# Kernel optimization log

Measured on AMD Instinct MI355X. Metric: run time of the kernel, lower is better.

The kernel has to match this reference:

```python
import jax, jax.numpy as jnp
import numpy as np

NUM_HEADS = 4
NUM_GROUPS = 8
EPS = 1e-5


def setup_inputs() -> dict:
    key = jax.random.key(0)
    ks = jax.random.split(key, 4)
    b, c, h, w = 16, 512, 32, 32
    x = jax.random.normal(ks[0], (b, c, h, w), dtype=jnp.float32)
    norm_gamma = jnp.ones((c,), dtype=jnp.float32)
    norm_beta = jnp.zeros((c,), dtype=jnp.float32)
    qkv_w = jax.random.normal(ks[1], (3 * c, c), dtype=jnp.float32) * (c ** -0.5)
    qkv_b = jnp.zeros((3 * c,), dtype=jnp.float32)
    proj_w = jax.random.normal(ks[2], (c, c), dtype=jnp.float32) * (c ** -0.5)
    proj_b = jnp.zeros((c,), dtype=jnp.float32)
    return {"x": x, "norm_gamma": norm_gamma, "norm_beta": norm_beta,
            "qkv_w": qkv_w, "qkv_b": qkv_b, "proj_w": proj_w, "proj_b": proj_b}


def reference(x, norm_gamma, norm_beta, qkv_w, qkv_b, proj_w, proj_b):
    b, c, h, w = x.shape
    nh = NUM_HEADS
    dh = c // nh
    n = h * w
    # GroupNorm(8, c): normalize over (c/G, h, w) within each group, biased var
    xg = x.reshape(b, NUM_GROUPS, -1)
    mu = jnp.mean(xg, axis=-1, keepdims=True)
    var = jnp.var(xg, axis=-1, keepdims=True)
    xn = ((xg - mu) * jax.lax.rsqrt(var + EPS)).reshape(b, c, h, w)
    xn = xn * norm_gamma[:, None, None] + norm_beta[:, None, None]
    # QKV 1x1 conv == channel matmul
    qkv = jnp.einsum('oc,bchw->bohw', qkv_w, xn) + qkv_b[:, None, None]
    q, k, v = jnp.split(qkv, 3, axis=1)  # each [b, c, h, w]

    def to_heads(t):  # [b, c, h, w] -> [b, nh, n, dh]
        return t.reshape(b, nh, dh, n).transpose(0, 1, 3, 2)

    q, k, v = to_heads(q), to_heads(k), to_heads(v)
    scale = dh ** -0.5
    attn = jax.nn.softmax(jnp.einsum('bhnd,bhmd->bhnm', q, k) * scale, axis=-1)
    out = jnp.einsum('bhnm,bhmd->bhnd', attn, v)  # [b, nh, n, dh]
    out = out.transpose(0, 1, 3, 2).reshape(b, c, h, w)
    out = jnp.einsum('oc,bchw->bohw', proj_w, out) + proj_b[:, None, None]
    return x + out
```

## Files before the change

### kernel.cpp

```cpp
#include <hip/hip_runtime.h>

typedef unsigned short u16;
typedef unsigned int   u32;

typedef __attribute__((ext_vector_type(8)))  short bf16x8;
typedef __attribute__((ext_vector_type(16))) float f32x16;
typedef __attribute__((ext_vector_type(2)))  unsigned int u32x2;
#define MFMA32(a, b, c) __builtin_amdgcn_mfma_f32_32x32x16_bf16(a, b, c, 0, 0, 0)

__device__ __forceinline__ float bf2f(u16 h) { return __uint_as_float(((u32)h) << 16); }
__device__ __forceinline__ u16 f2bf(float f) {
  u32 u = __float_as_uint(f);
  u += 0x7fffu + ((u >> 16) & 1u);
  return (u16)(u >> 16);
}
__device__ __forceinline__ void unpack8(uint4 u, float* f) {
  f[0] = __uint_as_float(u.x << 16); f[1] = __uint_as_float(u.x & 0xffff0000u);
  f[2] = __uint_as_float(u.y << 16); f[3] = __uint_as_float(u.y & 0xffff0000u);
  f[4] = __uint_as_float(u.z << 16); f[5] = __uint_as_float(u.z & 0xffff0000u);
  f[6] = __uint_as_float(u.w << 16); f[7] = __uint_as_float(u.w & 0xffff0000u);
}
__device__ __forceinline__ void unpack4(uint2 u, float* f) {
  f[0] = __uint_as_float(u.x << 16); f[1] = __uint_as_float(u.x & 0xffff0000u);
  f[2] = __uint_as_float(u.y << 16); f[3] = __uint_as_float(u.y & 0xffff0000u);
}

template <bool F>
__device__ __forceinline__ void load8(const void* p, size_t idx, float* f) {
  if constexpr (F) {
    const float4* q = (const float4*)((const float*)p + idx);
    float4 a = q[0], b = q[1];
    f[0] = a.x; f[1] = a.y; f[2] = a.z; f[3] = a.w;
    f[4] = b.x; f[5] = b.y; f[6] = b.z; f[7] = b.w;
  } else {
    unpack8(*(const uint4*)((const u16*)p + idx), f);
  }
}
template <bool F>
__device__ __forceinline__ void load4(const void* p, size_t idx, float* f) {
  if constexpr (F) {
    float4 a = *(const float4*)((const float*)p + idx);
    f[0] = a.x; f[1] = a.y; f[2] = a.z; f[3] = a.w;
  } else {
    unpack4(*(const uint2*)((const u16*)p + idx), f);
  }
}
template <bool F>
__device__ __forceinline__ float load1(const void* p, size_t idx) {
  if constexpr (F) return ((const float*)p)[idx];
  else return bf2f(((const u16*)p)[idx]);
}

__device__ __forceinline__ void gl2lds16(const void* g, void* l) {
  __builtin_amdgcn_global_load_lds(
      (const __attribute__((address_space(1))) void*)g,
      (__attribute__((address_space(3))) void*)l, 16, 0, 0);
}

__global__ void detect_dtype(const void* __restrict__ x, int* __restrict__ flag) {
  if (threadIdx.x == 0 && blockIdx.x == 0) {
    const u32* p = (const u32*)x;
    int sane = 0;
    for (int i = 0; i < 256; ++i) {
      u32 e = (p[i] >> 7) & 0xFFu;
      sane += (e >= 100u && e <= 150u) ? 1 : 0;
    }
    *flag = (sane < 192) ? 1 : 0;
  }
}

__global__ void signal_ws(u16* __restrict__ out, int n) {
  int i = blockIdx.x * 256 + threadIdx.x;
  if (i < n) out[i] = 0x42C8;
}

#define SM_SCALE 0.08838834764831843f
#define QSC 0.12751743f


__global__ void __launch_bounds__(256) wconv_rt(const void* __restrict__ qkvw,
                                                const void* __restrict__ qkvb,
                                                u16* __restrict__ dst,
                                                const int* __restrict__ flag) {
  const bool F = (flag[0] != 0);
  int i = (blockIdx.x * 256 + threadIdx.x) * 8;
  if (i >= 787968) return;
  if (!F) {
    uint4 v = (i < 786432) ? *(const uint4*)((const u16*)qkvw + i)
                           : *(const uint4*)((const u16*)qkvb + (i - 786432));
    *(uint4*)(dst + i) = v;
  } else {
    const float* src = (i < 786432) ? ((const float*)qkvw + i)
                                    : ((const float*)qkvb + (i - 786432));
    float f[8];
    float4 a = *(const float4*)src, b = *(const float4*)(src + 4);
    f[0]=a.x; f[1]=a.y; f[2]=a.z; f[3]=a.w; f[4]=b.x; f[5]=b.y; f[6]=b.z; f[7]=b.w;
    u32 w0 = (u32)f2bf(f[0]) | ((u32)f2bf(f[1]) << 16);
    u32 w1 = (u32)f2bf(f[2]) | ((u32)f2bf(f[3]) << 16);
    u32 w2 = (u32)f2bf(f[4]) | ((u32)f2bf(f[5]) << 16);
    u32 w3 = (u32)f2bf(f[6]) | ((u32)f2bf(f[7]) << 16);
    *(uint4*)(dst + i) = make_uint4(w0, w1, w2, w3);
  }
}

template <bool F>
__device__ __forceinline__ void gn_stats2_body(const void* __restrict__ x,
                                               float* __restrict__ part,
                                               int g, int b, int half, int tid,
                                               float* ssum, float* ssq) {
  const size_t base = (size_t)(b * 512 + g * 64 + half * 32) * 1024;
  float sum = 0.f, sq = 0.f;
  for (int i = tid; i < 4096; i += 256) {
    float f[8]; load8<F>(x, base + (size_t)i * 8, f);
#pragma unroll
    for (int m = 0; m < 8; ++m) { sum += f[m]; sq += f[m] * f[m]; }
  }
  ssum[tid] = sum; ssq[tid] = sq; __syncthreads();
  for (int off = 128; off > 0; off >>= 1) {
    if (tid < off) { ssum[tid] += ssum[tid + off]; ssq[tid] += ssq[tid + off]; }
    __syncthreads();
  }
  if (tid == 0) {
    part[(b * 8 + g) * 4 + half * 2 + 0] = ssum[0];
    part[(b * 8 + g) * 4 + half * 2 + 1] = ssq[0];
  }
}

__global__ void __launch_bounds__(256) gn_stats2(const void* __restrict__ x,
                                                 float* __restrict__ part,
                                                 const int* __restrict__ flag) {
  __shared__ float ssum[256], ssq[256];
  const int g = blockIdx.x, b = blockIdx.y, half = blockIdx.z, tid = threadIdx.x;
  if (flag[0] != 0) gn_stats2_body<true >(x, part, g, b, half, tid, ssum, ssq);
  else              gn_stats2_body<false>(x, part, g, b, half, tid, ssum, ssq);
}

template <bool F>
__device__ __forceinline__ void gn_apply_body(
    const void* __restrict__ x, const void* __restrict__ gamma,
    const void* __restrict__ beta, const float* __restrict__ part,
    u16* __restrict__ xT, int chunk, int b, int tid,
    float* scb, float* bsb, float (*Tf)[64][65]) {
  const int s0 = chunk * 64;
  for (int c = tid; c < 512; c += 256) {
    int gg = c >> 6;
    const float* p = part + (b * 8 + gg) * 4;
    float sum = p[0] + p[2], sq = p[1] + p[3];
    float mu  = sum * (1.f / 65536.f);
    float var = sq * (1.f / 65536.f) - mu * mu;
    float s = load1<F>(gamma, c) * rsqrtf(var + 1e-5f);
    scb[c] = s;
    bsb[c] = load1<F>(beta, c) - mu * s;
  }
  __syncthreads();

  for (int gb = 0; gb < 8; ++gb) {
    const int pb = gb & 1;
#pragma unroll
    for (int half = 0; half < 2; ++half) {
      int idx = tid + half * 256;
      int c_loc = idx >> 3, s8 = (idx & 7) * 8;
      int c = gb * 64 + c_loc;
      float f[8];
      load8<F>(x, (size_t)(b * 512 + c) * 1024 + s0 + s8, f);
      float sm = scb[c], ba = bsb[c];
#pragma unroll
      for (int m = 0; m < 8; ++m) Tf[pb][s8 + m][c_loc] = f[m] * sm + ba;
    }
    __syncthreads();
#pragma unroll
    for (int half = 0; half < 2; ++half) {
      int idx = tid + half * 256;
      int s_loc = idx >> 3, c8 = (idx & 7) * 8;
      u32 pk[4];
#pragma unroll
      for (int m = 0; m < 4; ++m)
        pk[m] = (u32)f2bf(Tf[pb][s_loc][c8 + 2 * m]) |
                ((u32)f2bf(Tf[pb][s_loc][c8 + 2 * m + 1]) << 16);
      *(uint4*)(xT + (size_t)(b * 1024 + s0 + s_loc) * 512 + gb * 64 + c8) =
          make_uint4(pk[0], pk[1], pk[2], pk[3]);
    }
  }
}

__global__ void __launch_bounds__(256) gn_apply(const void* __restrict__ x,
                                                const void* __restrict__ gamma,
                                                const void* __restrict__ beta,
                                                const float* __restrict__ part,
                                                u16* __restrict__ xT,
                                                const int* __restrict__ flag) {
  __shared__ float scb[512], bsb[512];
  __shared__ float Tf[2][64][65];
  const int chunk = blockIdx.x, b = blockIdx.y, tid = threadIdx.x;
  if (flag[0] != 0) gn_apply_body<true >(x, gamma, beta, part, xT, chunk, b, tid, scb, bsb, Tf);
  else              gn_apply_body<false>(x, gamma, beta, part, xT, chunk, b, tid, scb, bsb, Tf);
}

__global__ void __launch_bounds__(256, 4)
gemm_qkv(const u16* __restrict__ xT, const u16* __restrict__ wbf,
         u16* __restrict__ qkT, u16* __restrict__ Vbuf) {
  const bool vrole = (blockIdx.y >= 8);
  const int n0 = blockIdx.x * 128;
  const int m0 = (vrole ? (int)blockIdx.y - 8 : (int)blockIdx.y) * 128;
  const int b  = blockIdx.z;
  __shared__ __align__(16) u16 At[8192];
  __shared__ __align__(16) u16 Bt[8192];
  const int tid = threadIdx.x;
  const int w = tid >> 6, lane = tid & 63;
  const int lo = lane & 31, hi = lane >> 5;
  const int wm = w >> 1, wn = w & 1;
  const u16* bias = wbf + 786432;
  const u16* Ab = vrole ? (wbf + 524288) : (xT + (size_t)b * 524288);
  const u16* Bb = vrole ? (xT + (size_t)b * 524288) : wbf;
  u16* outp = vrole ? (Vbuf + (size_t)b * 524288) : (qkT + (size_t)b * 1048576);
  const int srow = lane >> 3, spc = lane & 7;

  f32x16 cA[2][2];
#pragma unroll
  for (int i = 0; i < 2; ++i)
#pragma unroll
    for (int j = 0; j < 2; ++j)
#pragma unroll
      for (int r = 0; r < 16; ++r) cA[i][j][r] = 0.f;

  for (int kt = 0; kt < 8; ++kt) {
    const int kb = kt * 64;
#pragma unroll
    for (int c = 0; c < 4; ++c) {
      int grp = w * 4 + c;
      int row = grp * 8 + srow;
      int lc  = spc ^ (row & 7);
      gl2lds16(Ab + (size_t)(m0 + row) * 512 + kb + lc * 8, &At[grp * 512]);
      gl2lds16(Bb + (size_t)(n0 + row) * 512 + kb + lc * 8, &Bt[grp * 512]);
    }
    __syncthreads();
#pragma unroll
    for (int k16 = 0; k16 < 4; ++k16) {
      const int lc = k16 * 2 + hi;
      const int rA0 = wm * 64 + lo,  rA1 = rA0 + 32;
      const int rB0 = wn * 64 + lo,  rB1 = rB0 + 32;
      bf16x8 a0 = *(const bf16x8*)&At[rA0 * 64 + ((lc ^ (rA0 & 7)) << 3)];
      bf16x8 a1 = *(const bf16x8*)&At[rA1 * 64 + ((lc ^ (rA1 & 7)) << 3)];
      bf16x8 b0 = *(const bf16x8*)&Bt[rB0 * 64 + ((lc ^ (rB0 & 7)) << 3)];
      bf16x8 b1 = *(const bf16x8*)&Bt[rB1 * 64 + ((lc ^ (rB1 & 7)) << 3)];
      cA[0][0] = MFMA32(a0, b0, cA[0][0]);
      cA[0][1] = MFMA32(a0, b1, cA[0][1]);
      cA[1][0] = MFMA32(a1, b0, cA[1][0]);
      cA[1][1] = MFMA32(a1, b1, cA[1][1]);
    }
    __syncthreads();
  }

  float bcol[2] = {0.f, 0.f};
  if (!vrole) {
    bcol[0] = bf2f(bias[n0 + wn * 64 + lo]);
    bcol[1] = bf2f(bias[n0 + wn * 64 + 32 + lo]);
  }
#pragma unroll
  for (int mt = 0; mt < 2; ++mt)
#pragma unroll
    for (int nt = 0; nt < 2; ++nt) {
      const int nbase = n0 + wn * 64 + nt * 32;
#pragma unroll
      for (int r = 0; r < 16; ++r) {
        int m = m0 + wm * 64 + mt * 32 + (r & 3) + 8 * (r >> 2) + 4 * hi;
        int n = nbase + lo;
        float v = cA[mt][nt][r];
        if (!vrole) {
          v += bcol[nt];
          if (nbase < 512) v *= QSC;
        } else {
          v += bf2f(bias[1024 + m]);
        }
        outp[(size_t)m * 1024 + n] = f2bf(v);
      }
    }
}

template <bool F>
__device__ __forceinline__ void proj_body(const void* __restrict__ A,
                                          const u16* __restrict__ B,
                                          const void* __restrict__ bias,
                                          const void* __restrict__ resid,
                                          void* __restrict__ outp,
                                          int n0, int m0, int b, int tid,
                                          u16 (*At)[72], u16 (*Bt)[72]) {
  const int w = tid >> 6, lane = tid & 63;
  const int lo = lane & 31, hi = lane >> 5;
  const int wm = w >> 1, wn = w & 1;
  const size_t bBase = (size_t)b * 524288;

  f32x16 cA[2][2];
#pragma unroll
  for (int i = 0; i < 2; ++i)
#pragma unroll
    for (int j = 0; j < 2; ++j)
#pragma unroll
      for (int r = 0; r < 16; ++r) cA[i][j][r] = 0.f;

  for (int kt = 0; kt < 8; ++kt) {
#pragma unroll
    for (int i = 0; i < 4; ++i) {
      int idx = tid + i * 256;
      int row = idx >> 3, kc = (idx & 7) * 8;
      int k = kt * 64 + kc;
      {
        if constexpr (F) {
          float f[8]; load8<true>(A, (size_t)(m0 + row) * 512 + k, f);
          u32 w0 = (u32)f2bf(f[0]) | ((u32)f2bf(f[1]) << 16);
          u32 w1 = (u32)f2bf(f[2]) | ((u32)f2bf(f[3]) << 16);
          u32 w2 = (u32)f2bf(f[4]) | ((u32)f2bf(f[5]) << 16);
          u32 w3 = (u32)f2bf(f[6]) | ((u32)f2bf(f[7]) << 16);
          *(uint4*)&At[row][kc] = make_uint4(w0, w1, w2, w3);
        } else {
          *(uint4*)&At[row][kc] =
              *(const uint4*)((const u16*)A + (size_t)(m0 + row) * 512 + k);
        }
      }
      *(uint4*)&Bt[row][kc] =
          *(const uint4*)(B + bBase + (size_t)(n0 + row) * 512 + k);
    }
    __syncthreads();
#pragma unroll
    for (int k16 = 0; k16 < 4; ++k16) {
      const int ko = k16 * 16 + hi * 8;
      bf16x8 a0 = *(const bf16x8*)&At[wm * 64 + lo][ko];
      bf16x8 a1 = *(const bf16x8*)&At[wm * 64 + 32 + lo][ko];
      bf16x8 b0 = *(const bf16x8*)&Bt[wn * 64 + lo][ko];
      bf16x8 b1 = *(const bf16x8*)&Bt[wn * 64 + 32 + lo][ko];
      cA[0][0] = MFMA32(a0, b0, cA[0][0]);
      cA[0][1] = MFMA32(a0, b1, cA[0][1]);
      cA[1][0] = MFMA32(a1, b0, cA[1][0]);
      cA[1][1] = MFMA32(a1, b1, cA[1][1]);
    }
    __syncthreads();
  }

#pragma unroll
  for (int mt = 0; mt < 2; ++mt)
#pragma unroll
    for (int nt = 0; nt < 2; ++nt) {
#pragma unroll
      for (int r = 0; r < 16; ++r) {
        int m = m0 + wm * 64 + mt * 32 + (r & 3) + 8 * (r >> 2) + 4 * hi;
        int n = n0 + wn * 64 + nt * 32 + lo;
        float v = cA[mt][nt][r];
        v += load1<F>(bias, m);
        v += load1<F>(resid, bBase + (size_t)m * 1024 + n);
        size_t off = bBase + (size_t)m * 1024 + n;
        if constexpr (F) ((float*)outp)[off] = v;
        else             ((u16*)outp)[off] = f2bf(v);
      }
    }
}

__global__ void __launch_bounds__(256, 4)
proj_rt(const void* __restrict__ projw, const u16* __restrict__ aout,
        const void* __restrict__ projb, const void* __restrict__ x,
        void* __restrict__ outp, const int* __restrict__ flag) {
  __shared__ __align__(16) u16 At[128][72];
  __shared__ __align__(16) u16 Bt[128][72];
  const int n0 = blockIdx.x * 128, m0 = blockIdx.y * 128, b = blockIdx.z;
  if (flag[0] != 0) proj_body<true >(projw, aout, projb, x, outp, n0, m0, b, threadIdx.x, At, Bt);
  else              proj_body<false>(projw, aout, projb, x, outp, n0, m0, b, threadIdx.x, At, Bt);
}

__global__ void __launch_bounds__(256, 2) attn4(const u16* __restrict__ qkT,
                                                const u16* __restrict__ V,
                                                u16* __restrict__ aout) {
  const int bh = blockIdx.x;
  const int q0 = blockIdx.y * 128;
  const int b = bh >> 2, h = bh & 3;
  const u16* qt = qkT + (size_t)b * 1048576;
  const u16* vb = V + (size_t)b * 524288 + (size_t)(h * 128) * 1024;
  __shared__ __align__(16) u16 smem[32768];
  const int tid = threadIdx.x;
  const int w = tid >> 6, lane = tid & 63;
  const int lo = lane & 31, hi = lane >> 5;

#pragma unroll
  for (int c = 0; c < 8; ++c) {
    int grp = w * 8 + c;
    int row = grp * 4 + (lane >> 4);
    int lc  = (lane & 15) ^ (row & 7);
    gl2lds16(qt + (size_t)(q0 + row) * 1024 + h * 128 + lc * 8, &smem[grp * 512]);
  }
#pragma unroll
  for (int c = 0; c < 4; ++c) {
    int grp = w * 4 + c;
    { int row = grp * 4 + (lane >> 4);
      int lc  = (lane & 15) ^ (row & 7);
      gl2lds16(qt + (size_t)row * 1024 + 512 + h * 128 + lc * 8,
               &smem[16384 + grp * 512]); }
    { int row = grp * 8 + (lane >> 3);
      int lc  = (lane & 7) ^ (row & 7);
      gl2lds16(vb + (size_t)row * 1024 + lc * 8,
               &smem[16384 + 8192 + grp * 512]); }
  }
  __syncthreads();
  bf16x8 qf[8];
  {
    const int row = 32 * w + lo;
#pragma unroll
    for (int k16 = 0; k16 < 8; ++k16) {
      int lc = k16 * 2 + hi;
      qf[k16] = *(const bf16x8*)&smem[row * 128 + ((lc ^ (row & 7)) << 3)];
    }
  }
  __syncthreads();

  f32x16 o[4];
  float lp = 0.f;
#pragma unroll
  for (int dt = 0; dt < 4; ++dt)
#pragma unroll
    for (int r = 0; r < 16; ++r) o[dt][r] = 0.f;

  for (int kt = 0; kt < 16; ++kt) {
    const u16* rb = &smem[((kt & 1) ^ 1) << 14];
    u16* wbuf = &smem[(kt & 1) << 14];

    if (kt < 15) {
      const int k0n = (kt + 1) * 64;
#pragma unroll
      for (int c = 0; c < 4; ++c) {
        int grp = w * 4 + c;
        { int row = grp * 4 + (lane >> 4);
          int lc  = (lane & 15) ^ (row & 7);
          gl2lds16(qt + (size_t)(k0n + row) * 1024 + 512 + h * 128 + lc * 8,
                   wbuf + grp * 512); }
        { int row = grp * 8 + (lane >> 3);
          int lc  = (lane & 7) ^ (row & 7);
          gl2lds16(vb + (size_t)row * 1024 + k0n + lc * 8,
                   wbuf + 8192 + grp * 512); }
      }
    }

    f32x16 s0, s1;
#pragma unroll
    for (int r = 0; r < 16; ++r) { s0[r] = 0.f; s1[r] = 0.f; }
#pragma unroll
    for (int k16 = 0; k16 < 8; ++k16) {
      const int lc = k16 * 2 + hi;
      const int r0 = lo, r1 = lo + 32;
      bf16x8 kf0 = *(const bf16x8*)&rb[r0 * 128 + ((lc ^ (r0 & 7)) << 3)];
      bf16x8 kf1 = *(const bf16x8*)&rb[r1 * 128 + ((lc ^ (r1 & 7)) << 3)];
      s0 = MFMA32(kf0, qf[k16], s0);
      s1 = MFMA32(kf1, qf[k16], s1);
    }

#pragma unroll
    for (int r = 0; r < 16; ++r) {
      s0[r] = exp2f(s0[r]);
      s1[r] = exp2f(s1[r]);
      lp += s0[r] + s1[r];
    }

    bf16x8 pa[4];
#define MKPA(ps, rb0, dst) do {                                               \
      u32 qa0, qa1, qb0, qb1;                                                 \
      asm("v_cvt_pk_bf16_f32 %0, %1, %2" : "=v"(qa0)                          \
          : "v"((ps)[(rb0) + 0]), "v"((ps)[(rb0) + 1]));                      \
      asm("v_cvt_pk_bf16_f32 %0, %1, %2" : "=v"(qa1)                          \
          : "v"((ps)[(rb0) + 2]), "v"((ps)[(rb0) + 3]));                      \
      asm("v_cvt_pk_bf16_f32 %0, %1, %2" : "=v"(qb0)                          \
          : "v"((ps)[(rb0) + 4]), "v"((ps)[(rb0) + 5]));                      \
      asm("v_cvt_pk_bf16_f32 %0, %1, %2" : "=v"(qb1)                          \
          : "v"((ps)[(rb0) + 6]), "v"((ps)[(rb0) + 7]));                      \
      u32x2 r0 = __builtin_amdgcn_permlane32_swap(qa0, qb0, false, false);    \
      u32x2 r1 = __builtin_amdgcn_permlane32_swap(qa1, qb1, false, false);    \
      union { u32 u[4]; bf16x8 v8; } pk_;                                     \
      pk_.u[0] = r0[0]; pk_.u[1] = r1[0]; pk_.u[2] = r0[1]; pk_.u[3] = r1[1]; \
      dst = pk_.v8;                                                           \
    } while (0)
    MKPA(s0, 0, pa[0]);
    MKPA(s0, 8, pa[1]);
    MKPA(s1, 0, pa[2]);
    MKPA(s1, 8, pa[3]);
#undef MKPA

#pragma unroll
    for (int t = 0; t < 4; ++t) {
      const int lc = t * 2 + hi;
#pragma unroll
      for (int dt = 0; dt < 4; ++dt) {
        const int row = dt * 32 + lo;
        bf16x8 bv = *(const bf16x8*)&rb[8192 + row * 64 + ((lc ^ (row & 7)) << 3)];
        o[dt] = MFMA32(pa[t], bv, o[dt]);
      }
    }
    __syncthreads();
  }

  float linv = 1.f / (lp + __shfl_xor(lp, 32));
#pragma unroll
  for (int r = 0; r < 16; ++r) {
    int pat = (r & 3) + 8 * (r >> 2) + 4 * hi;
    float lr = __shfl(linv, pat);
    int q = q0 + 32 * w + pat;
    size_t base = (size_t)(b * 1024 + q) * 512 + h * 128;
    aout[base +  0 + lo] = f2bf(o[0][r] * lr);
    aout[base + 32 + lo] = f2bf(o[1][r] * lr);
    aout[base + 64 + lo] = f2bf(o[2][r] * lr);
    aout[base + 96 + lo] = f2bf(o[3][r] * lr);
  }
}


template <bool F>
__global__ void __launch_bounds__(256) gn_stats(const void* __restrict__ x,
                                                const void* __restrict__ gamma,
                                                const void* __restrict__ beta,
                                                float* __restrict__ sc,
                                                float* __restrict__ bs,
                                                const int* __restrict__ flag) {
  if ((flag[0] != 0) != F) return;
  const int g = blockIdx.x, b = blockIdx.y;
  const int tid = threadIdx.x;
  const size_t base = (size_t)(b * 512 + g * 64) * 1024;
  float sum = 0.f, sq = 0.f;
  for (int i = tid; i < 8192; i += 256) {
    float f[8]; load8<F>(x, base + (size_t)i * 8, f);
#pragma unroll
    for (int m = 0; m < 8; ++m) { sum += f[m]; sq += f[m] * f[m]; }
  }
  __shared__ float ssum[256], ssq[256];
  ssum[tid] = sum; ssq[tid] = sq; __syncthreads();
  for (int off = 128; off > 0; off >>= 1) {
    if (tid < off) { ssum[tid] += ssum[tid + off]; ssq[tid] += ssq[tid + off]; }
    __syncthreads();
  }
  if (tid < 64) {
    float mu  = ssum[0] * (1.f / 65536.f);
    float var = ssq[0] * (1.f / 65536.f) - mu * mu;
    int c = g * 64 + tid;
    float s = load1<F>(gamma, c) * rsqrtf(var + 1e-5f);
    sc[b * 512 + c] = s;
    bs[b * 512 + c] = load1<F>(beta, c) - mu * s;
  }
}

template <bool F, bool BEXT, bool FOUT>
__global__ void __launch_bounds__(256) gemm64(const void* __restrict__ A,
                                              const void* __restrict__ B,
                                              const float* __restrict__ sc,
                                              const float* __restrict__ bs,
                                              const void* __restrict__ bias,
                                              const void* __restrict__ resid,
                                              void* __restrict__ outp,
                                              int mrows, int donorm, int bstride,
                                              const int* __restrict__ flag) {
  if ((flag[0] != 0) != F) return;
  const int s0 = blockIdx.x * 64;
  const int o0 = blockIdx.y * 64;
  const int b  = blockIdx.z;
  __shared__ __align__(16) float At[64][36];
  __shared__ __align__(16) float Bt[64][36];
  const int tid = threadIdx.x;
  const int ty = tid >> 4, tx = tid & 15;
  const int i0 = ty * 4, j0 = tx * 4;
  const int arow = tid >> 2, akc = (tid & 3) * 8;
  const int brow = tid >> 3, bnc = (tid & 7) * 8;
  float acc[4][4] = {};

  for (int kt = 0; kt < 512; kt += 32) {
    float af[8];
    load8<F>(A, (size_t)(o0 + arow) * 512 + akc + kt, af);
    *(float4*)&At[arow][akc]     = make_float4(af[0], af[1], af[2], af[3]);
    *(float4*)&At[arow][akc + 4] = make_float4(af[4], af[5], af[6], af[7]);
    const int c = kt + brow;
    float bf[8];
    load8<(BEXT && F)>(B, (size_t)(b * bstride + c) * 1024 + s0 + bnc, bf);
    float smul = 1.f, badd = 0.f;
    if (donorm) { smul = sc[b * 512 + c]; badd = bs[b * 512 + c]; }
#pragma unroll
    for (int m = 0; m < 8; ++m) Bt[bnc + m][brow] = bf[m] * smul + badd;
    __syncthreads();
#pragma unroll
    for (int kq = 0; kq < 8; ++kq) {
      float4 a0 = *(const float4*)&At[i0 + 0][kq * 4];
      float4 a1 = *(const float4*)&At[i0 + 1][kq * 4];
      float4 a2 = *(const float4*)&At[i0 + 2][kq * 4];
      float4 a3 = *(const float4*)&At[i0 + 3][kq * 4];
      float4 c0 = *(const float4*)&Bt[j0 + 0][kq * 4];
      float4 c1 = *(const float4*)&Bt[j0 + 1][kq * 4];
      float4 c2 = *(const float4*)&Bt[j0 + 2][kq * 4];
      float4 c3 = *(const float4*)&Bt[j0 + 3][kq * 4];
#define DOT4(ii, jj, AV, CV) acc[ii][jj] += AV.x * CV.x + AV.y * CV.y + AV.z * CV.z + AV.w * CV.w;
      DOT4(0,0,a0,c0) DOT4(0,1,a0,c1) DOT4(0,2,a0,c2) DOT4(0,3,a0,c3)
      DOT4(1,0,a1,c0) DOT4(1,1,a1,c1) DOT4(1,2,a1,c2) DOT4(1,3,a1,c3)
      DOT4(2,0,a2,c0) DOT4(2,1,a2,c1) DOT4(2,2,a2,c2) DOT4(2,3,a2,c3)
      DOT4(3,0,a3,c0) DOT4(3,1,a3,c1) DOT4(3,2,a3,c2) DOT4(3,3,a3,c3)
#undef DOT4
    }
    __syncthreads();
  }
#pragma unroll
  for (int ii = 0; ii < 4; ++ii) {
    const int o = o0 + i0 + ii;
    const float bb = load1<F>(bias, o);
    float v[4];
#pragma unroll
    for (int jj = 0; jj < 4; ++jj) v[jj] = acc[ii][jj] + bb;
    if (resid) {
      float xf[4];
      load4<F>(resid, (size_t)(b * 512 + o) * 1024 + s0 + j0, xf);
#pragma unroll
      for (int jj = 0; jj < 4; ++jj) v[jj] += xf[jj];
    }
    const size_t ooff = (size_t)(b * mrows + o) * 1024 + s0 + j0;
    if constexpr (FOUT) {
      *(float4*)((float*)outp + ooff) = make_float4(v[0], v[1], v[2], v[3]);
    } else {
      uint2 pk;
      pk.x = (u32)f2bf(v[0]) | ((u32)f2bf(v[1]) << 16);
      pk.y = (u32)f2bf(v[2]) | ((u32)f2bf(v[3]) << 16);
      *(uint2*)((u16*)outp + ooff) = pk;
    }
  }
}

__global__ void __launch_bounds__(256, 2) attn_old(u16* __restrict__ qkv) {
  const int q0 = blockIdx.x * 128;
  const int bh = blockIdx.y;
  const int b = bh >> 2, h = bh & 3;
  u16* qp = qkv + (size_t)(b * 1536 + h * 128) * 1024;
  const u16* kp = qp + (size_t)512 * 1024;
  const u16* vp = qp + (size_t)1024 * 1024;
  __shared__ __align__(16) u16 Qt[128][136];
  __shared__ __align__(16) u16 Kt[32][136];
  __shared__ __align__(16) u16 Vt[128][40];
  __shared__ __align__(16) u16 Pt[128][40];
  const int tid = threadIdx.x;
  const int w = tid >> 6, lane = tid & 63;
  const int lo = lane & 31, hi = lane >> 5;

  for (int idx = tid; idx < 2048; idx += 256) {
    int d = idx >> 4, s8 = (idx & 15) * 8;
    uint4 qv = *(const uint4*)(qp + (size_t)d * 1024 + q0 + s8);
    const u16* qs = (const u16*)&qv;
#pragma unroll
    for (int m = 0; m < 8; ++m) Qt[s8 + m][d] = qs[m];
  }
  __syncthreads();
  bf16x8 qf[8];
#pragma unroll
  for (int kq = 0; kq < 8; ++kq)
    qf[kq] = *(const bf16x8*)&Qt[32 * w + lo][kq * 16 + hi * 8];

  f32x16 o0, o1, o2, o3;
  float lp[16];
#pragma unroll
  for (int r = 0; r < 16; ++r) { o0[r] = 0.f; o1[r] = 0.f; o2[r] = 0.f; o3[r] = 0.f; lp[r] = 0.f; }

  for (int kt = 0; kt < 32; ++kt) {
    const int k0 = kt * 32;
    __syncthreads();
    for (int idx = tid; idx < 512; idx += 256) {
      int d = idx >> 2, s8 = (idx & 3) * 8;
      uint4 kv = *(const uint4*)(kp + (size_t)d * 1024 + k0 + s8);
      const u16* ks = (const u16*)&kv;
#pragma unroll
      for (int m = 0; m < 8; ++m) Kt[s8 + m][d] = ks[m];
      *(uint4*)&Vt[d][s8] = *(const uint4*)(vp + (size_t)d * 1024 + k0 + s8);
    }
    __syncthreads();
    f32x16 acc;
#pragma unroll
    for (int r = 0; r < 16; ++r) acc[r] = 0.f;
#pragma unroll
    for (int kq = 0; kq < 8; ++kq) {
      bf16x8 bq = *(const bf16x8*)&Kt[lo][kq * 16 + hi * 8];
      acc = MFMA32(qf[kq], bq, acc);
    }
#pragma unroll
    for (int r = 0; r < 16; ++r) {
      float pe = __expf(acc[r] * SM_SCALE);
      lp[r] += pe;
      int row = (r & 3) + 8 * (r >> 2) + 4 * hi;
      Pt[32 * w + row][lo] = f2bf(pe);
    }
    __syncthreads();
#pragma unroll
    for (int kq2 = 0; kq2 < 2; ++kq2) {
      bf16x8 a2 = *(const bf16x8*)&Pt[32 * w + lo][kq2 * 16 + hi * 8];
      bf16x8 b0 = *(const bf16x8*)&Vt[ 0 + lo][kq2 * 16 + hi * 8];
      bf16x8 b1 = *(const bf16x8*)&Vt[32 + lo][kq2 * 16 + hi * 8];
      bf16x8 b2 = *(const bf16x8*)&Vt[64 + lo][kq2 * 16 + hi * 8];
      bf16x8 b3 = *(const bf16x8*)&Vt[96 + lo][kq2 * 16 + hi * 8];
      o0 = MFMA32(a2, b0, o0);
      o1 = MFMA32(a2, b1, o1);
      o2 = MFMA32(a2, b2, o2);
      o3 = MFMA32(a2, b3, o3);
    }
  }
#pragma unroll
  for (int r = 0; r < 16; ++r) {
    float su = lp[r];
    su += __shfl_xor(su, 1);  su += __shfl_xor(su, 2);
    su += __shfl_xor(su, 4);  su += __shfl_xor(su, 8);
    su += __shfl_xor(su, 16);
    float linv = 1.f / su;
    int row = (r & 3) + 8 * (r >> 2) + 4 * hi;
    int q = q0 + 32 * w + row;
    size_t base = (size_t)(b * 1536 + h * 128) * 1024 + q;
    qkv[base + (size_t)( 0 + lo) * 1024] = f2bf(o0[r] * linv);
    qkv[base + (size_t)(32 + lo) * 1024] = f2bf(o1[r] * linv);
    qkv[base + (size_t)(64 + lo) * 1024] = f2bf(o2[r] * linv);
    qkv[base + (size_t)(96 + lo) * 1024] = f2bf(o3[r] * linv);
  }
}

extern "C" void kernel_launch(void* const* d_in, const int* in_sizes, int n_in,
                              void* d_out, int out_size, void* d_ws, size_t ws_size,
                              hipStream_t stream) {
  const void* x     = d_in[0];
  const void* gamma = d_in[1];
  const void* beta  = d_in[2];
  const void* qkvw  = d_in[3];
  const void* qkvb  = d_in[4];
  const void* projw = d_in[5];
  const void* projb = d_in[6];

  char* ws = (char*)d_ws;
  const size_t MB = 1024 * 1024;
  const size_t FAST_NEED = 64 * MB + 64;
  const size_t OLD_NEED  = 48 * MB + 256 + 2 * 16 * 512 * 4;

  if (ws_size >= FAST_NEED) {
    u16* xT   = (u16*)ws;
    u16* qkT  = (u16*)(ws + 16 * MB);
    u16* Vbuf = (u16*)(ws + 48 * MB);
    int* flag = (int*)(ws + 64 * MB);
    u16* wbf  = (u16*)d_out;
    float* part = (float*)((char*)d_out + 2 * MB);

    detect_dtype<<<1, 64, 0, stream>>>(x, flag);
    wconv_rt<<<385, 256, 0, stream>>>(qkvw, qkvb, wbf, flag);
    gn_stats2<<<dim3(8, 16, 2), 256, 0, stream>>>(x, part, flag);
    gn_apply<<<dim3(16, 16), 256, 0, stream>>>(x, gamma, beta, part, xT, flag);

    gemm_qkv<<<dim3(8, 12, 16), 256, 0, stream>>>(xT, wbf, qkT, Vbuf);

    attn4<<<dim3(64, 8), 256, 0, stream>>>(qkT, Vbuf, xT);

    proj_rt<<<dim3(8, 4, 16), 256, 0, stream>>>(projw, xT, projb, x, d_out, flag);
    return;
  }

  if (ws_size < OLD_NEED) {
    signal_ws<<<(out_size + 255) / 256, 256, 0, stream>>>((u16*)d_out, out_size);
    return;
  }

  const size_t QKV_BYTES = (size_t)16 * 1536 * 1024 * 2;
  u16* qkv  = (u16*)ws;
  int* flag = (int*)(ws + QKV_BYTES);
  float* sc = (float*)(ws + QKV_BYTES + 256);
  float* bs = sc + 16 * 512;

  detect_dtype<<<1, 64, 0, stream>>>(x, flag);
  gn_stats<false><<<dim3(8, 16), 256, 0, stream>>>(x, gamma, beta, sc, bs, flag);
  gn_stats<true ><<<dim3(8, 16), 256, 0, stream>>>(x, gamma, beta, sc, bs, flag);
  gemm64<false, true, false><<<dim3(16, 24, 16), 256, 0, stream>>>(
      qkvw, x, sc, bs, qkvb, nullptr, qkv, 1536, 1, 512, flag);
  gemm64<true, true, false><<<dim3(16, 24, 16), 256, 0, stream>>>(
      qkvw, x, sc, bs, qkvb, nullptr, qkv, 1536, 1, 512, flag);
  attn_old<<<dim3(8, 64), 256, 0, stream>>>(qkv);
  gemm64<false, false, false><<<dim3(16, 8, 16), 256, 0, stream>>>(
      projw, qkv, sc, bs, projb, x, d_out, 512, 0, 1536, flag);
  gemm64<true, false, true><<<dim3(16, 8, 16), 256, 0, stream>>>(
      projw, qkv, sc, bs, projb, x, d_out, 512, 0, 1536, flag);
}
```

Before: 237.7 us.

## Merge prep kernels, detect dtype per block, and split gn_apply across channel groups

Removes the single-thread detect_dtype launch and the global flag. Each block now checks the dtype itself by sampling 256 words of x with a shared-memory reduction. Weight conversion and GroupNorm statistics are merged into one prep kernel of 641 blocks. gn_apply gains a z dimension of 4 so each block handles 128 channels instead of 512, giving four times as many blocks. Together these cut two launches and the serial flag dependency, at the cost of a small reduction and extra barriers in every block.

```diff
diff --git a/kernel.cpp b/kernel.cpp
--- a/kernel.cpp
+++ b/kernel.cpp
@@ -57,6 +57,20 @@
       (__attribute__((address_space(3))) void*)l, 16, 0, 0);
 }
 
+__device__ __forceinline__ bool blk_is_f32(const void* x, int tid, int* sh) {
+  const u32* p = (const u32*)x;
+  u32 e = (p[tid] >> 7) & 0xFFu;
+  sh[tid] = (e >= 100u && e <= 150u) ? 1 : 0;
+  __syncthreads();
+  for (int off = 128; off > 0; off >>= 1) {
+    if (tid < off) sh[tid] += sh[tid + off];
+    __syncthreads();
+  }
+  bool r = sh[0] < 192;
+  __syncthreads();
+  return r;
+}
+
 __global__ void detect_dtype(const void* __restrict__ x, int* __restrict__ flag) {
   if (threadIdx.x == 0 && blockIdx.x == 0) {
     const u32* p = (const u32*)x;
@@ -78,92 +92,93 @@
 #define QSC 0.12751743f
 
 
-__global__ void __launch_bounds__(256) wconv_rt(const void* __restrict__ qkvw,
-                                                const void* __restrict__ qkvb,
-                                                u16* __restrict__ dst,
-                                                const int* __restrict__ flag) {
-  const bool F = (flag[0] != 0);
-  int i = (blockIdx.x * 256 + threadIdx.x) * 8;
-  if (i >= 787968) return;
-  if (!F) {
-    uint4 v = (i < 786432) ? *(const uint4*)((const u16*)qkvw + i)
-                           : *(const uint4*)((const u16*)qkvb + (i - 786432));
-    *(uint4*)(dst + i) = v;
+__global__ void __launch_bounds__(256) prep_rt(const void* __restrict__ x,
+                                               const void* __restrict__ qkvw,
+                                               const void* __restrict__ qkvb,
+                                               u16* __restrict__ wdst,
+                                               float* __restrict__ part) {
+  __shared__ float ssum[256], ssq[256];
+  __shared__ int sfl[256];
+  const int tid = threadIdx.x;
+  const bool F = blk_is_f32(x, tid, sfl);
+  const int bx = blockIdx.x;
+
+  if (bx < 256) {
+    const int g = bx & 7, b = (bx >> 3) & 15, half = bx >> 7;
+    const size_t base = (size_t)(b * 512 + g * 64 + half * 32) * 1024;
+    float sum = 0.f, sq = 0.f;
+    if (F) {
+      for (int i = tid; i < 4096; i += 256) {
+        float f[8]; load8<true>(x, base + (size_t)i * 8, f);
+#pragma unroll
+        for (int m = 0; m < 8; ++m) { sum += f[m]; sq += f[m] * f[m]; }
+      }
+    } else {
+      for (int i = tid; i < 4096; i += 256) {
+        float f[8]; load8<false>(x, base + (size_t)i * 8, f);
+#pragma unroll
+        for (int m = 0; m < 8; ++m) { sum += f[m]; sq += f[m] * f[m]; }
+      }
+    }
+    ssum[tid] = sum; ssq[tid] = sq; __syncthreads();
+    for (int off = 128; off > 0; off >>= 1) {
+      if (tid < off) { ssum[tid] += ssum[tid + off]; ssq[tid] += ssq[tid + off]; }
+      __syncthreads();
+    }
+    if (tid == 0) {
+      part[(b * 8 + g) * 4 + half * 2 + 0] = ssum[0];
+      part[(b * 8 + g) * 4 + half * 2 + 1] = ssq[0];
+    }
   } else {
-    const float* src = (i < 786432) ? ((const float*)qkvw + i)
-                                    : ((const float*)qkvb + (i - 786432));
-    float f[8];
-    float4 a = *(const float4*)src, b = *(const float4*)(src + 4);
-    f[0]=a.x; f[1]=a.y; f[2]=a.z; f[3]=a.w; f[4]=b.x; f[5]=b.y; f[6]=b.z; f[7]=b.w;
-    u32 w0 = (u32)f2bf(f[0]) | ((u32)f2bf(f[1]) << 16);
-    u32 w1 = (u32)f2bf(f[2]) | ((u32)f2bf(f[3]) << 16);
-    u32 w2 = (u32)f2bf(f[4]) | ((u32)f2bf(f[5]) << 16);
-    u32 w3 = (u32)f2bf(f[6]) | ((u32)f2bf(f[7]) << 16);
-    *(uint4*)(dst + i) = make_uint4(w0, w1, w2, w3);
-  }
-}
-
-template <bool F>
-__device__ __forceinline__ void gn_stats2_body(const void* __restrict__ x,
-                                               float* __restrict__ part,
-                                               int g, int b, int half, int tid,
-                                               float* ssum, float* ssq) {
-  const size_t base = (size_t)(b * 512 + g * 64 + half * 32) * 1024;
-  float sum = 0.f, sq = 0.f;
-  for (int i = tid; i < 4096; i += 256) {
-    float f[8]; load8<F>(x, base + (size_t)i * 8, f);
-#pragma unroll
-    for (int m = 0; m < 8; ++m) { sum += f[m]; sq += f[m] * f[m]; }
-  }
-  ssum[tid] = sum; ssq[tid] = sq; __syncthreads();
-  for (int off = 128; off > 0; off >>= 1) {
-    if (tid < off) { ssum[tid] += ssum[tid + off]; ssq[tid] += ssq[tid + off]; }
-    __syncthreads();
-  }
-  if (tid == 0) {
-    part[(b * 8 + g) * 4 + half * 2 + 0] = ssum[0];
-    part[(b * 8 + g) * 4 + half * 2 + 1] = ssq[0];
-  }
-}
-
-__global__ void __launch_bounds__(256) gn_stats2(const void* __restrict__ x,
-                                                 float* __restrict__ part,
-                                                 const int* __restrict__ flag) {
-  __shared__ float ssum[256], ssq[256];
-  const int g = blockIdx.x, b = blockIdx.y, half = blockIdx.z, tid = threadIdx.x;
-  if (flag[0] != 0) gn_stats2_body<true >(x, part, g, b, half, tid, ssum, ssq);
-  else              gn_stats2_body<false>(x, part, g, b, half, tid, ssum, ssq);
+    int i = ((bx - 256) * 256 + tid) * 8;
+    if (i >= 787968) return;
+    if (!F) {
+      uint4 v = (i < 786432) ? *(const uint4*)((const u16*)qkvw + i)
+                             : *(const uint4*)((const u16*)qkvb + (i - 786432));
+      *(uint4*)(wdst + i) = v;
+    } else {
+      const float* src = (i < 786432) ? ((const float*)qkvw + i)
+                                      : ((const float*)qkvb + (i - 786432));
+      float4 a = *(const float4*)src, b4 = *(const float4*)(src + 4);
+      u32 w0 = (u32)f2bf(a.x) | ((u32)f2bf(a.y) << 16);
+      u32 w1 = (u32)f2bf(a.z) | ((u32)f2bf(a.w) << 16);
+      u32 w2 = (u32)f2bf(b4.x) | ((u32)f2bf(b4.y) << 16);
+      u32 w3 = (u32)f2bf(b4.z) | ((u32)f2bf(b4.w) << 16);
+      *(uint4*)(wdst + i) = make_uint4(w0, w1, w2, w3);
+    }
+  }
 }
 
 template <bool F>
 __device__ __forceinline__ void gn_apply_body(
     const void* __restrict__ x, const void* __restrict__ gamma,
     const void* __restrict__ beta, const float* __restrict__ part,
-    u16* __restrict__ xT, int chunk, int b, int tid,
+    u16* __restrict__ xT, int chunk, int b, int z, int tid,
     float* scb, float* bsb, float (*Tf)[64][65]) {
   const int s0 = chunk * 64;
-  for (int c = tid; c < 512; c += 256) {
-    int gg = c >> 6;
+  if (tid < 128) {
+    int gg = z * 2 + (tid >> 6);
     const float* p = part + (b * 8 + gg) * 4;
     float sum = p[0] + p[2], sq = p[1] + p[3];
     float mu  = sum * (1.f / 65536.f);
     float var = sq * (1.f / 65536.f) - mu * mu;
+    int c = z * 128 + tid;
     float s = load1<F>(gamma, c) * rsqrtf(var + 1e-5f);
-    scb[c] = s;
-    bsb[c] = load1<F>(beta, c) - mu * s;
+    scb[tid] = s;
+    bsb[tid] = load1<F>(beta, c) - mu * s;
   }
   __syncthreads();
 
-  for (int gb = 0; gb < 8; ++gb) {
+  for (int gb = 0; gb < 2; ++gb) {
     const int pb = gb & 1;
 #pragma unroll
     for (int half = 0; half < 2; ++half) {
       int idx = tid + half * 256;
       int c_loc = idx >> 3, s8 = (idx & 7) * 8;
-      int c = gb * 64 + c_loc;
+      int c = (z * 2 + gb) * 64 + c_loc;
       float f[8];
       load8<F>(x, (size_t)(b * 512 + c) * 1024 + s0 + s8, f);
-      float sm = scb[c], ba = bsb[c];
+      float sm = scb[gb * 64 + c_loc], ba = bsb[gb * 64 + c_loc];
 #pragma unroll
       for (int m = 0; m < 8; ++m) Tf[pb][s8 + m][c_loc] = f[m] * sm + ba;
     }
@@ -177,8 +192,8 @@
       for (int m = 0; m < 4; ++m)
         pk[m] = (u32)f2bf(Tf[pb][s_loc][c8 + 2 * m]) |
                 ((u32)f2bf(Tf[pb][s_loc][c8 + 2 * m + 1]) << 16);
-      *(uint4*)(xT + (size_t)(b * 1024 + s0 + s_loc) * 512 + gb * 64 + c8) =
-          make_uint4(pk[0], pk[1], pk[2], pk[3]);
+      *(uint4*)(xT + (size_t)(b * 1024 + s0 + s_loc) * 512 +
+                (z * 2 + gb) * 64 + c8) = make_uint4(pk[0], pk[1], pk[2], pk[3]);
     }
   }
 }
@@ -187,13 +202,14 @@
                                                 const void* __restrict__ gamma,
                                                 const void* __restrict__ beta,
                                                 const float* __restrict__ part,
-                                                u16* __restrict__ xT,
-                                                const int* __restrict__ flag) {
-  __shared__ float scb[512], bsb[512];
+                                                u16* __restrict__ xT) {
+  __shared__ float scb[128], bsb[128];
   __shared__ float Tf[2][64][65];
-  const int chunk = blockIdx.x, b = blockIdx.y, tid = threadIdx.x;
-  if (flag[0] != 0) gn_apply_body<true >(x, gamma, beta, part, xT, chunk, b, tid, scb, bsb, Tf);
-  else              gn_apply_body<false>(x, gamma, beta, part, xT, chunk, b, tid, scb, bsb, Tf);
+  __shared__ int sfl[256];
+  const int chunk = blockIdx.x, b = blockIdx.y, z = blockIdx.z, tid = threadIdx.x;
+  const bool F = blk_is_f32(x, tid, sfl);
+  if (F) gn_apply_body<true >(x, gamma, beta, part, xT, chunk, b, z, tid, scb, bsb, Tf);
+  else   gn_apply_body<false>(x, gamma, beta, part, xT, chunk, b, z, tid, scb, bsb, Tf);
 }
 
 __global__ void __launch_bounds__(256, 4)
@@ -357,12 +373,14 @@
 __global__ void __launch_bounds__(256, 4)
 proj_rt(const void* __restrict__ projw, const u16* __restrict__ aout,
         const void* __restrict__ projb, const void* __restrict__ x,
-        void* __restrict__ outp, const int* __restrict__ flag) {
+        void* __restrict__ outp) {
   __shared__ __align__(16) u16 At[128][72];
   __shared__ __align__(16) u16 Bt[128][72];
+  __shared__ int sfl[256];
   const int n0 = blockIdx.x * 128, m0 = blockIdx.y * 128, b = blockIdx.z;
-  if (flag[0] != 0) proj_body<true >(projw, aout, projb, x, outp, n0, m0, b, threadIdx.x, At, Bt);
-  else              proj_body<false>(projw, aout, projb, x, outp, n0, m0, b, threadIdx.x, At, Bt);
+  const bool F = blk_is_f32(x, threadIdx.x, sfl);
+  if (F) proj_body<true >(projw, aout, projb, x, outp, n0, m0, b, threadIdx.x, At, Bt);
+  else   proj_body<false>(projw, aout, projb, x, outp, n0, m0, b, threadIdx.x, At, Bt);
 }
 
 __global__ void __launch_bounds__(256, 2) attn4(const u16* __restrict__ qkT,
@@ -731,20 +749,17 @@
     u16* xT   = (u16*)ws;
     u16* qkT  = (u16*)(ws + 16 * MB);
     u16* Vbuf = (u16*)(ws + 48 * MB);
-    int* flag = (int*)(ws + 64 * MB);
     u16* wbf  = (u16*)d_out;
     float* part = (float*)((char*)d_out + 2 * MB);
 
-    detect_dtype<<<1, 64, 0, stream>>>(x, flag);
-    wconv_rt<<<385, 256, 0, stream>>>(qkvw, qkvb, wbf, flag);
-    gn_stats2<<<dim3(8, 16, 2), 256, 0, stream>>>(x, part, flag);
-    gn_apply<<<dim3(16, 16), 256, 0, stream>>>(x, gamma, beta, part, xT, flag);
+    prep_rt<<<641, 256, 0, stream>>>(x, qkvw, qkvb, wbf, part);
+    gn_apply<<<dim3(16, 16, 4), 256, 0, stream>>>(x, gamma, beta, part, xT);
 
     gemm_qkv<<<dim3(8, 12, 16), 256, 0, stream>>>(xT, wbf, qkT, Vbuf);
 
     attn4<<<dim3(64, 8), 256, 0, stream>>>(qkT, Vbuf, xT);
 
-    proj_rt<<<dim3(8, 4, 16), 256, 0, stream>>>(projw, xT, projb, x, d_out, flag);
+    proj_rt<<<dim3(8, 4, 16), 256, 0, stream>>>(projw, xT, projb, x, d_out);
     return;
   }
 
```

After: 225.7 us. 1.05x faster.
